# Kernel tuning notes

Hardware: AMD Instinct MI355X
Metric: run time of the kernel (lower is better)

Reference implementation:

```python
import jax, jax.numpy as jnp
import numpy as np

N_NODES = 50000
N_EDGES = 300000
HID = 256


def setup_inputs() -> dict:
    key = jax.random.key(0)
    ks = jax.random.split(key, 8)
    s = lambda fan_in: 1.0 / np.sqrt(fan_in)
    return {
        "node_embeddings": jax.random.normal(ks[0], (N_NODES, HID), dtype=jnp.float32),
        "edge_index": jax.random.randint(ks[1], (2, N_EDGES), 0, N_NODES, dtype=jnp.int64),
        "edge_attr": jax.random.normal(ks[2], (N_EDGES, 3), dtype=jnp.float32),
        "W1": jax.random.normal(ks[3], (2 * HID + 3, HID), dtype=jnp.float32) * s(2 * HID + 3),
        "b1": jnp.zeros((HID,), dtype=jnp.float32),
        "W2": jax.random.normal(ks[4], (HID, HID // 2), dtype=jnp.float32) * s(HID),
        "b2": jnp.zeros((HID // 2,), dtype=jnp.float32),
        "W3": jax.random.normal(ks[5], (HID // 2, HID // 4), dtype=jnp.float32) * s(HID // 2),
        "b3": jnp.zeros((HID // 4,), dtype=jnp.float32),
        "W4": jax.random.normal(ks[6], (HID // 4, 3), dtype=jnp.float32) * s(HID // 4),
        "b4": jnp.zeros((3,), dtype=jnp.float32),
    }


def reference(node_embeddings, edge_index, edge_attr, W1, b1, W2, b2, W3, b3, W4, b4):
    # Gather source/target node embeddings: [E, H] each
    src = node_embeddings[edge_index[0]]
    dst = node_embeddings[edge_index[1]]
    feats = jnp.concatenate([src, dst, edge_attr], axis=-1)  # [E, 2H+3]
    # edge_encoder: Linear -> ReLU -> (Dropout=identity in eval) -> Linear
    h = jax.nn.relu(feats @ W1 + b1)
    h = h @ W2 + b2  # [E, H//2]
    # classifier: Linear -> ReLU -> Linear
    h = jax.nn.relu(h @ W3 + b3)
    logits = h @ W4 + b4  # [E, 3]
    return logits
```

## Files before the change

kernel.cpp:

```cpp
#include <hip/hip_runtime.h>
#include <hip/hip_bf16.h>
#include <stdint.h>
#include <stddef.h>


#define NN 50000
#define NE 300000
#define KG(kq,g2) ((kq)*2+(g2))
#define NBG1 391

using bf16x8 = __attribute__((ext_vector_type(8))) short;
using f32x16 = __attribute__((ext_vector_type(16))) float;
using f32x4  = __attribute__((ext_vector_type(4))) float;
using f32x2  = __attribute__((ext_vector_type(2))) float;
using u32x4  = __attribute__((ext_vector_type(4))) unsigned int;
using u32x2  = __attribute__((ext_vector_type(2))) unsigned int;

#define OFF_PQ   0ULL
#define SZ_PQ    (50000ULL*512ULL*2ULL)
#define OFF_W1   (OFF_PQ + SZ_PQ)
#define SZ_W1    (512ULL*256ULL*2ULL)
#define OFF_W1C  (OFF_W1 + SZ_W1)
#define SZ_W1C   (3ULL*256ULL*4ULL)
#define OFF_W2   (OFF_W1C + SZ_W1C)
#define SZ_W2    (128ULL*256ULL*2ULL)
#define OFF_W3   (OFF_W2 + SZ_W2)
#define SZ_W3    (64ULL*128ULL*2ULL)
#define OFF_W4   (OFF_W3 + SZ_W3)
#define SZ_W4    (16ULL*64ULL*2ULL)
#define OFF_FLAG (OFF_W4 + SZ_W4)
#define WS_NEED  (OFF_FLAG + 16ULL)

__device__ __forceinline__ unsigned short f2bf(float x){
  unsigned u = __float_as_uint(x);
  unsigned r = 0x7FFFu + ((u >> 16) & 1u);
  return (unsigned short)((u + r) >> 16);
}
__device__ __forceinline__ unsigned cvtpk(float lo, float hi){
  unsigned r;
  asm("v_cvt_pk_bf16_f32 %0, %1, %2" : "=v"(r) : "v"(lo), "v"(hi));
  return r;
}
__device__ __forceinline__ f32x2 unpk(unsigned w){
  f32x2 r;
  r[0] = __uint_as_float(w << 16);
  r[1] = __uint_as_float(w & 0xFFFF0000u);
  return r;
}
__device__ __forceinline__ f32x16 mfma32(bf16x8 a, bf16x8 b, f32x16 c){
  return __builtin_amdgcn_mfma_f32_32x32x16_bf16(a, b, c, 0, 0, 0);
}
__device__ __forceinline__ f32x4 mfma16(bf16x8 a, bf16x8 b, f32x4 c){
  return __builtin_amdgcn_mfma_f32_16x16x32_bf16(a, b, c, 0, 0, 0);
}
__device__ __forceinline__ f32x16 zero16(){
  f32x16 v;
#pragma unroll
  for (int i = 0; i < 16; ++i) v[i] = 0.f;
  return v;
}

__global__ void prep_pack(const float* __restrict__ W1,
                          const int* __restrict__ ei32, char* __restrict__ ws)
{
  int i = blockIdx.x * 256 + threadIdx.x;
  unsigned short* w1i = (unsigned short*)(ws + OFF_W1);
  if (i < 131072){
    int out = i & 511;
    int kgj = i >> 9;
    int kg = kgj >> 3, j = kgj & 7;
    int k = (kg >> 1)*16 + (kg & 1)*8 + j;
    float v = (out < 256) ? W1[(size_t)k*256 + out]
                          : W1[(size_t)(256 + k)*256 + (out - 256)];
    w1i[((size_t)kg*512 + out)*8 + j] = f2bf(v);
  }
  if (i == 0){
    int f = 1;
    for (int t = 1; t < 64; t += 2) if (ei32[t] != 0) { f = 0; break; }
    *(int*)(ws + OFF_FLAG) = f;
  }
}

__global__ __launch_bounds__(512, 2) void gemm1(const float* __restrict__ emb,
                                                const float* __restrict__ b1,
                                                const float* __restrict__ W1,
                                                const float* __restrict__ W2,
                                                const float* __restrict__ W3,
                                                const float* __restrict__ W4,
                                                char* __restrict__ ws)
{
  __shared__ __align__(16) unsigned short U[16896];

  const int tid = threadIdx.x;
  const int bid = blockIdx.x;

  if (bid >= NBG1){
    int p = (bid - NBG1)*512 + tid;
    unsigned short* w2i = (unsigned short*)(ws + OFF_W2);
    unsigned short* w3i = (unsigned short*)(ws + OFF_W3);
    unsigned short* w4i = (unsigned short*)(ws + OFF_W4);
    float* w1c = (float*)(ws + OFF_W1C);
    if (p < 32768){
      int j = p & 7, out = (p >> 3) & 127, sg = p >> 10;
      int k = (sg >> 2)*32 + (sg & 3)*8 + j;
      w2i[p] = f2bf(W2[(size_t)k*128 + out]);
    } else if (p < 40960){
      int i3 = p - 32768;
      int j = i3 & 7, out = (i3 >> 3) & 63, sg = i3 >> 9;
      int k = (sg >> 2)*32 + (sg & 3)*8 + j;
      w3i[i3] = f2bf(W3[(size_t)k*64 + out]);
    } else if (p < 41984){
      int i4 = p - 40960;
      int j = i4 & 7, out = (i4 >> 3) & 15, sg = i4 >> 7;
      int k = (sg >> 2)*32 + (sg & 3)*8 + j;
      w4i[i4] = (out < 3) ? f2bf(W4[(size_t)k*3 + out]) : (unsigned short)0;
    } else if (p < 42752){
      int i5 = p - 41984;
      w1c[i5] = W1[(size_t)(512 + i5/256)*256 + (i5 & 255)];
    }
    return;
  }

  const int wv = tid >> 6, l = tid & 63, ln = l & 31, g2 = l >> 5;
  const int ob = wv * 64;
  const unsigned short* w1L = (const unsigned short*)(ws + OFF_W1);
  unsigned short* PQ = (unsigned short*)(ws + OFF_PQ);

  bf16x8 aw[2][16];
#pragma unroll
  for (int kq = 0; kq < 16; ++kq){
#pragma unroll
    for (int t2 = 0; t2 < 2; ++t2)
      aw[t2][kq] = *(const bf16x8*)(w1L + ((size_t)KG(kq,g2)*512 + ob + t2*32 + ln)*8);
  }

#pragma unroll 1
  for (int rep = 0; rep < 2; ++rep){
    const int nb = (bid*2 + rep) * 64;
    __syncthreads();

#pragma unroll
    for (int it = 0; it < 8; ++it){
      int u = it*512 + tid;
      int kg = u >> 7, node = (u >> 1) & 63, half = u & 1;
      int n = nb + node; if (n >= NN) n = NN - 1;
      int k = (kg >> 1)*16 + (kg & 1)*8 + half*4;
      f32x4 e = *(const f32x4*)(emb + (size_t)n*256 + k);
      u32x2 w; w[0] = cvtpk(e[0], e[1]); w[1] = cvtpk(e[2], e[3]);
      *(u32x2*)(U + (size_t)kg*512 + node*8 + half*4) = w;
    }
    __syncthreads();

    f32x16 acc[2][2];
    acc[0][0] = zero16(); acc[0][1] = zero16();
    acc[1][0] = zero16(); acc[1][1] = zero16();
#pragma unroll
    for (int kq = 0; kq < 16; ++kq){
      bf16x8 b0  = *(const bf16x8*)(U + ((size_t)KG(kq,g2)*64 +      ln)*8);
      bf16x8 b1v = *(const bf16x8*)(U + ((size_t)KG(kq,g2)*64 + 32 + ln)*8);
      acc[0][0] = mfma32(aw[0][kq], b0,  acc[0][0]);
      acc[1][0] = mfma32(aw[1][kq], b0,  acc[1][0]);
      acc[0][1] = mfma32(aw[0][kq], b1v, acc[0][1]);
      acc[1][1] = mfma32(aw[1][kq], b1v, acc[1][1]);
    }
    __syncthreads();

    const int r_ = tid >> 4;
    const int j_ = tid & 15;
#define G1PASS(BG)                                                             \
    {                                                                          \
      _Pragma("unroll")                                                        \
      for (int t2 = 0; t2 < 2; ++t2){                                          \
        _Pragma("unroll")                                                      \
        for (int rr = 0; rr < 4; ++rr){                                        \
          int o = ob + t2*32 + rr*8 + g2*4;                                    \
          f32x4 bv = {0.f,0.f,0.f,0.f};                                        \
          if (ob + t2*32 < 256) bv = *(const f32x4*)(b1 + o);                  \
          unsigned d0 = cvtpk(acc[t2][BG][rr*4+0]+bv[0], acc[t2][BG][rr*4+1]+bv[1]); \
          unsigned d1 = cvtpk(acc[t2][BG][rr*4+2]+bv[2], acc[t2][BG][rr*4+3]+bv[3]); \
          u32x2 st = {d0, d1};                                                 \
          *(u32x2*)(U + (size_t)ln*516 + o) = st;                              \
        }                                                                      \
      }                                                                        \
      __syncthreads();                                                         \
      {                                                                        \
        int n = nb + (BG)*32 + r_;                                             \
        if (n < NN){                                                           \
          _Pragma("unroll")                                                    \
          for (int ii = 0; ii < 4; ++ii){                                      \
            uint4 v = *(const uint4*)(U + (size_t)r_*516 + ii*128 + j_*8);     \
            *(uint4*)(PQ + (size_t)n*512 + ii*128 + j_*8) = v;                 \
          }                                                                    \
        }                                                                      \
      }                                                                        \
    }
    G1PASS(0);
    __syncthreads();
    G1PASS(1);
#undef G1PASS
  }
}


#define PAIRX(LO, HI, D) ((D)==0 ? (f32x2){(LO)[0],(LO)[1]} : \
                          (D)==1 ? (f32x2){(LO)[2],(LO)[3]} : \
                          (D)==2 ? (f32x2){(HI)[0],(HI)[1]} : \
                                   (f32x2){(HI)[2],(HI)[3]})

#define H1BUILD(PC, QC, A0, A1, A2, BOUT)                                      \
  {                                                                            \
    u32x4 pu = __builtin_bit_cast(u32x4, PC);                                  \
    u32x4 qu = __builtin_bit_cast(u32x4, QC);                                  \
    f32x2 z2 = {0.f, 0.f};                                                     \
    unsigned bu0, bu1, bu2, bu3;                                               \
    _Pragma("unroll")                                                          \
    for (int d = 0; d < 4; ++d){                                               \
      f32x2 h = unpk(pu[d]) + unpk(qu[d]);                                     \
      h += PAIRX(w0lo, w0hi, d) * (A0);                                        \
      h += PAIRX(w1lo, w1hi, d) * (A1);                                        \
      h += PAIRX(w2lo, w2hi, d) * (A2);                                        \
      h = __builtin_elementwise_max(h, z2);                                    \
      unsigned c = cvtpk(h[0], h[1]);                                          \
      if (d==0) bu0 = c; else if (d==1) bu1 = c; else if (d==2) bu2 = c;       \
      else bu3 = c;                                                            \
    }                                                                          \
    u32x4 buv = {bu0, bu1, bu2, bu3};                                          \
    BOUT = __builtin_bit_cast(bf16x8, buv);                                    \
  }

#define L2S(S, P0, Q0, P1, Q1)                                                 \
  {                                                                            \
    const int kb = (S)*32 + g4*8;                                              \
    f32x4 w0lo = *(const f32x4*)(w1c_lds +   0 + kb);                          \
    f32x4 w0hi = *(const f32x4*)(w1c_lds +   4 + kb);                          \
    f32x4 w1lo = *(const f32x4*)(w1c_lds + 256 + kb);                          \
    f32x4 w1hi = *(const f32x4*)(w1c_lds + 260 + kb);                          \
    f32x4 w2lo = *(const f32x4*)(w1c_lds + 512 + kb);                          \
    f32x4 w2hi = *(const f32x4*)(w1c_lds + 516 + kb);                          \
    bf16x8 b0, b1;                                                             \
    H1BUILD(P0, Q0, at0e0, at1e0, at2e0, b0);                                  \
    H1BUILD(P1, Q1, at0e1, at1e1, at2e1, b1);                                  \
    if ((S) + 2 <= 7){                                                         \
      P0 = *(const bf16x8*)(Prow0 + ((S)+2)*32);                               \
      Q0 = *(const bf16x8*)(Qrow0 + ((S)+2)*32);                               \
      P1 = *(const bf16x8*)(Prow1 + ((S)+2)*32);                               \
      Q1 = *(const bf16x8*)(Qrow1 + ((S)+2)*32);                               \
    }                                                                          \
    const char* abase = smem + (size_t)((S)*4 + g4)*2048 + c16*16;             \
    _Pragma("unroll")                                                          \
    for (int t = 0; t < 8; ++t){                                               \
      bf16x8 af = *(const bf16x8*)(abase + t*256);                             \
      acc2[t][0] = mfma16(af, b0, acc2[t][0]);                                 \
      acc2[t][1] = mfma16(af, b1, acc2[t][1]);                                 \
    }                                                                          \
  }

__global__ __launch_bounds__(512, 4) void fused(const int* __restrict__ eidx,
                                                const float* __restrict__ attr,
                                                const float* __restrict__ b2,
                                                const float* __restrict__ b3,
                                                const float* __restrict__ b4,
                                                const char* __restrict__ ws,
                                                float* __restrict__ out)
{
  __shared__ __align__(16) char smem[65536 + 3072];
  const int tid = threadIdx.x;
  const int wv = tid >> 6, l = tid & 63, c16 = l & 15, g4 = l >> 4;

  const unsigned short* PQ  = (const unsigned short*)(ws + OFF_PQ);
  const unsigned short* w3g = (const unsigned short*)(ws + OFF_W3);
  const unsigned short* w4g = (const unsigned short*)(ws + OFF_W4);
  const float* W1c = (const float*)(ws + OFF_W1C);
  const int flag64 = *(const int*)(ws + OFF_FLAG);
  const float* w1c_lds = (const float*)(smem + 65536);

  const int ebase = blockIdx.x * 256 + wv * 32;
  const int e0 = ebase + c16,      e1 = ebase + 16 + c16;
  const bool ev0 = (e0 < NE),      ev1 = (e1 < NE);
  const int ec0 = ev0 ? e0 : 0,    ec1 = ev1 ? e1 : 0;
  const int si0 = flag64 ? eidx[2*(size_t)ec0]        : eidx[ec0];
  const int di0 = flag64 ? eidx[2*((size_t)NE + ec0)] : eidx[NE + ec0];
  const int si1 = flag64 ? eidx[2*(size_t)ec1]        : eidx[ec1];
  const int di1 = flag64 ? eidx[2*((size_t)NE + ec1)] : eidx[NE + ec1];

  const float at0e0 = ev0 ? attr[(size_t)ec0*3 + 0] : 0.f;
  const float at1e0 = ev0 ? attr[(size_t)ec0*3 + 1] : 0.f;
  const float at2e0 = ev0 ? attr[(size_t)ec0*3 + 2] : 0.f;
  const float at0e1 = ev1 ? attr[(size_t)ec1*3 + 0] : 0.f;
  const float at1e1 = ev1 ? attr[(size_t)ec1*3 + 1] : 0.f;
  const float at2e1 = ev1 ? attr[(size_t)ec1*3 + 2] : 0.f;

  const unsigned short* Prow0 = PQ + (size_t)si0*512 + g4*8;
  const unsigned short* Qrow0 = PQ + (size_t)di0*512 + 256 + g4*8;
  const unsigned short* Prow1 = PQ + (size_t)si1*512 + g4*8;
  const unsigned short* Qrow1 = PQ + (size_t)di1*512 + 256 + g4*8;

  bf16x8 pA0 = *(const bf16x8*)(Prow0 +  0), qA0 = *(const bf16x8*)(Qrow0 +  0);
  bf16x8 pA1 = *(const bf16x8*)(Prow1 +  0), qA1 = *(const bf16x8*)(Qrow1 +  0);
  bf16x8 pB0 = *(const bf16x8*)(Prow0 + 32), qB0 = *(const bf16x8*)(Qrow0 + 32);
  bf16x8 pB1 = *(const bf16x8*)(Prow1 + 32), qB1 = *(const bf16x8*)(Qrow1 + 32);

  {
    const uint4* src = (const uint4*)(ws + OFF_W2);
    uint4* dst = (uint4*)smem;
#pragma unroll
    for (int it = 0; it < 8; ++it) dst[it*512 + tid] = src[it*512 + tid];
    if (tid < 192) ((f32x4*)(smem + 65536))[tid] = ((const f32x4*)W1c)[tid];
  }
  __syncthreads();

  f32x4 acc2[8][2];
#pragma unroll
  for (int t = 0; t < 8; ++t){ acc2[t][0] = (f32x4){0,0,0,0}; acc2[t][1] = (f32x4){0,0,0,0}; }

  L2S(0, pA0, qA0, pA1, qA1);
  L2S(1, pB0, qB0, pB1, qB1);
  L2S(2, pA0, qA0, pA1, qA1);
  L2S(3, pB0, qB0, pB1, qB1);
  L2S(4, pA0, qA0, pA1, qA1);
  L2S(5, pB0, qB0, pB1, qB1);
  L2S(6, pA0, qA0, pA1, qA1);
  L2S(7, pB0, qB0, pB1, qB1);

  __syncthreads();

  unsigned short* hslot = (unsigned short*)(smem + wv*8192);
#pragma unroll
  for (int t = 0; t < 8; ++t){
    f32x4 bv = *(const f32x4*)(b2 + t*16 + g4*4);
    const int sg_o = t*2 + (g4 >> 1);
    const int j0 = (g4 & 1)*4;
#pragma unroll
    for (int g = 0; g < 2; ++g){
      unsigned d0 = cvtpk(acc2[t][g][0]+bv[0], acc2[t][g][1]+bv[1]);
      unsigned d1 = cvtpk(acc2[t][g][2]+bv[2], acc2[t][g][3]+bv[3]);
      u32x2 st = {d0, d1};
      *(u32x2*)(hslot + ((sg_o*32 + g*16 + c16)*8 + j0)) = st;
    }
  }

  f32x4 acc3[4][2];
#pragma unroll
  for (int t = 0; t < 4; ++t){ acc3[t][0] = (f32x4){0,0,0,0}; acc3[t][1] = (f32x4){0,0,0,0}; }
#pragma unroll
  for (int ks = 0; ks < 4; ++ks){
    const int sg = ks*4 + g4;
    bf16x8 bb0 = *(const bf16x8*)(hslot + (sg*32 +      c16)*8);
    bf16x8 bb1 = *(const bf16x8*)(hslot + (sg*32 + 16 + c16)*8);
#pragma unroll
    for (int t = 0; t < 4; ++t){
      bf16x8 af = *(const bf16x8*)(w3g + ((size_t)sg*64 + t*16 + c16)*8);
      acc3[t][0] = mfma16(af, bb0, acc3[t][0]);
      acc3[t][1] = mfma16(af, bb1, acc3[t][1]);
    }
  }

#pragma unroll
  for (int t = 0; t < 4; ++t){
    f32x4 bv = *(const f32x4*)(b3 + t*16 + g4*4);
    const int sg_o = t*2 + (g4 >> 1);
    const int j0 = (g4 & 1)*4;
#pragma unroll
    for (int g = 0; g < 2; ++g){
      unsigned d0 = cvtpk(fmaxf(acc3[t][g][0]+bv[0],0.f), fmaxf(acc3[t][g][1]+bv[1],0.f));
      unsigned d1 = cvtpk(fmaxf(acc3[t][g][2]+bv[2],0.f), fmaxf(acc3[t][g][3]+bv[3],0.f));
      u32x2 st = {d0, d1};
      *(u32x2*)(hslot + ((sg_o*32 + g*16 + c16)*8 + j0)) = st;
    }
  }

  f32x4 acc40 = {0,0,0,0}, acc41 = {0,0,0,0};
#pragma unroll
  for (int ks = 0; ks < 2; ++ks){
    const int sg = ks*4 + g4;
    bf16x8 af = *(const bf16x8*)(w4g + ((size_t)sg*16 + c16)*8);
    bf16x8 bb0 = *(const bf16x8*)(hslot + (sg*32 +      c16)*8);
    bf16x8 bb1 = *(const bf16x8*)(hslot + (sg*32 + 16 + c16)*8);
    acc40 = mfma16(af, bb0, acc40);
    acc41 = mfma16(af, bb1, acc41);
  }
  if (g4 == 0){
    float c0 = b4[0], c1 = b4[1], c2 = b4[2];
    if (ev0){
      out[(size_t)e0*3 + 0] = acc40[0] + c0;
      out[(size_t)e0*3 + 1] = acc40[1] + c1;
      out[(size_t)e0*3 + 2] = acc40[2] + c2;
    }
    if (ev1){
      out[(size_t)e1*3 + 0] = acc41[0] + c0;
      out[(size_t)e1*3 + 1] = acc41[1] + c1;
      out[(size_t)e1*3 + 2] = acc41[2] + c2;
    }
  }
}

extern "C" void kernel_launch(void* const* d_in, const int* in_sizes, int n_in,
                              void* d_out, int out_size, void* d_ws, size_t ws_size,
                              hipStream_t stream)
{
  const float* emb  = (const float*)d_in[0];
  const int*   eidx = (const int*)  d_in[1];
  const float* attr = (const float*)d_in[2];
  const float* W1   = (const float*)d_in[3];
  const float* b1   = (const float*)d_in[4];
  const float* W2   = (const float*)d_in[5];
  const float* b2   = (const float*)d_in[6];
  const float* W3   = (const float*)d_in[7];
  const float* b3   = (const float*)d_in[8];
  const float* W4   = (const float*)d_in[9];
  const float* b4   = (const float*)d_in[10];
  char* ws = (char*)d_ws;
  float* out = (float*)d_out;

  if (ws_size < WS_NEED) return;

  prep_pack<<<512, 256, 0, stream>>>(W1, eidx, ws);
  gemm1<<<NBG1 + 84, 512, 0, stream>>>(emb, b1, W1, W2, W3, W4, ws);
  fused<<<(NE + 255)/256, 512, 0, stream>>>(eidx, attr, b2, b3, b4, ws, out);
}
```

Measured before the change: 113.2 us.

## Process one node tile per block and stream W1 fragments to raise occupancy

The gemm1 kernel no longer preloads all 32 W1 fragments into registers and loops over two node tiles. Each block now handles a single 64-node tile, so there are twice as many blocks, and W1 fragments are double-buffered from global memory inside the unrolled MFMA loop. Launch bounds are raised to allow 4 blocks per CU. The goal is lower register pressure, higher occupancy and better latency hiding, at the cost of re-reading W1 from L2 for every block and losing reuse of the weights across tiles.

```diff
diff --git a/kernel.cpp b/kernel.cpp
--- a/kernel.cpp
+++ b/kernel.cpp
@@ -7,7 +7,7 @@
 #define NN 50000
 #define NE 300000
 #define KG(kq,g2) ((kq)*2+(g2))
-#define NBG1 391
+#define NBG1 782
 
 using bf16x8 = __attribute__((ext_vector_type(8))) short;
 using f32x16 = __attribute__((ext_vector_type(16))) float;
@@ -81,7 +81,7 @@
   }
 }
 
-__global__ __launch_bounds__(512, 2) void gemm1(const float* __restrict__ emb,
+__global__ __launch_bounds__(512, 4) void gemm1(const float* __restrict__ emb,
                                                 const float* __restrict__ b1,
                                                 const float* __restrict__ W1,
                                                 const float* __restrict__ W2,
@@ -123,82 +123,99 @@
 
   const int wv = tid >> 6, l = tid & 63, ln = l & 31, g2 = l >> 5;
   const int ob = wv * 64;
+  const int nb = bid * 64;
   const unsigned short* w1L = (const unsigned short*)(ws + OFF_W1);
   unsigned short* PQ = (unsigned short*)(ws + OFF_PQ);
 
-  bf16x8 aw[2][16];
-#pragma unroll
-  for (int kq = 0; kq < 16; ++kq){
-#pragma unroll
-    for (int t2 = 0; t2 < 2; ++t2)
-      aw[t2][kq] = *(const bf16x8*)(w1L + ((size_t)KG(kq,g2)*512 + ob + t2*32 + ln)*8);
-  }
-
-#pragma unroll 1
-  for (int rep = 0; rep < 2; ++rep){
-    const int nb = (bid*2 + rep) * 64;
-    __syncthreads();
-
-#pragma unroll
-    for (int it = 0; it < 8; ++it){
-      int u = it*512 + tid;
-      int kg = u >> 7, node = (u >> 1) & 63, half = u & 1;
-      int n = nb + node; if (n >= NN) n = NN - 1;
-      int k = (kg >> 1)*16 + (kg & 1)*8 + half*4;
-      f32x4 e = *(const f32x4*)(emb + (size_t)n*256 + k);
-      u32x2 w; w[0] = cvtpk(e[0], e[1]); w[1] = cvtpk(e[2], e[3]);
-      *(u32x2*)(U + (size_t)kg*512 + node*8 + half*4) = w;
-    }
-    __syncthreads();
-
-    f32x16 acc[2][2];
-    acc[0][0] = zero16(); acc[0][1] = zero16();
-    acc[1][0] = zero16(); acc[1][1] = zero16();
-#pragma unroll
-    for (int kq = 0; kq < 16; ++kq){
-      bf16x8 b0  = *(const bf16x8*)(U + ((size_t)KG(kq,g2)*64 +      ln)*8);
-      bf16x8 b1v = *(const bf16x8*)(U + ((size_t)KG(kq,g2)*64 + 32 + ln)*8);
-      acc[0][0] = mfma32(aw[0][kq], b0,  acc[0][0]);
-      acc[1][0] = mfma32(aw[1][kq], b0,  acc[1][0]);
-      acc[0][1] = mfma32(aw[0][kq], b1v, acc[0][1]);
-      acc[1][1] = mfma32(aw[1][kq], b1v, acc[1][1]);
-    }
-    __syncthreads();
-
-    const int r_ = tid >> 4;
-    const int j_ = tid & 15;
+#pragma unroll
+  for (int it = 0; it < 8; ++it){
+    int u = it*512 + tid;
+    int kg = u >> 7, node = (u >> 1) & 63, half = u & 1;
+    int n = nb + node; if (n >= NN) n = NN - 1;
+    int k = (kg >> 1)*16 + (kg & 1)*8 + half*4;
+    f32x4 e = *(const f32x4*)(emb + (size_t)n*256 + k);
+    u32x2 w; w[0] = cvtpk(e[0], e[1]); w[1] = cvtpk(e[2], e[3]);
+    *(u32x2*)(U + (size_t)kg*512 + node*8 + half*4) = w;
+  }
+
+  bf16x8 awA0 = *(const bf16x8*)(w1L + ((size_t)KG(0,g2)*512 + ob +      ln)*8);
+  bf16x8 awA1 = *(const bf16x8*)(w1L + ((size_t)KG(0,g2)*512 + ob + 32 + ln)*8);
+  bf16x8 awB0 = *(const bf16x8*)(w1L + ((size_t)KG(1,g2)*512 + ob +      ln)*8);
+  bf16x8 awB1 = *(const bf16x8*)(w1L + ((size_t)KG(1,g2)*512 + ob + 32 + ln)*8);
+
+  __syncthreads();
+
+  f32x16 acc[2][2];
+  acc[0][0] = zero16(); acc[0][1] = zero16();
+  acc[1][0] = zero16(); acc[1][1] = zero16();
+
+#define G1STEP(KQ, W0, W1F)                                                    \
+  {                                                                            \
+    bf16x8 b0  = *(const bf16x8*)(U + ((size_t)KG(KQ,g2)*64 +      ln)*8);     \
+    bf16x8 b1v = *(const bf16x8*)(U + ((size_t)KG(KQ,g2)*64 + 32 + ln)*8);     \
+    bf16x8 a0 = W0, a1 = W1F;                                                  \
+    if ((KQ) + 2 <= 15){                                                       \
+      W0  = *(const bf16x8*)(w1L + ((size_t)KG((KQ)+2,g2)*512 + ob +      ln)*8); \
+      W1F = *(const bf16x8*)(w1L + ((size_t)KG((KQ)+2,g2)*512 + ob + 32 + ln)*8); \
+    }                                                                          \
+    acc[0][0] = mfma32(a0, b0,  acc[0][0]);                                    \
+    acc[1][0] = mfma32(a1, b0,  acc[1][0]);                                    \
+    acc[0][1] = mfma32(a0, b1v, acc[0][1]);                                    \
+    acc[1][1] = mfma32(a1, b1v, acc[1][1]);                                    \
+  }
+  G1STEP(0,  awA0, awA1);
+  G1STEP(1,  awB0, awB1);
+  G1STEP(2,  awA0, awA1);
+  G1STEP(3,  awB0, awB1);
+  G1STEP(4,  awA0, awA1);
+  G1STEP(5,  awB0, awB1);
+  G1STEP(6,  awA0, awA1);
+  G1STEP(7,  awB0, awB1);
+  G1STEP(8,  awA0, awA1);
+  G1STEP(9,  awB0, awB1);
+  G1STEP(10, awA0, awA1);
+  G1STEP(11, awB0, awB1);
+  G1STEP(12, awA0, awA1);
+  G1STEP(13, awB0, awB1);
+  G1STEP(14, awA0, awA1);
+  G1STEP(15, awB0, awB1);
+#undef G1STEP
+
+  __syncthreads();
+
+  const int r_ = tid >> 4;
+  const int j_ = tid & 15;
 #define G1PASS(BG)                                                             \
+  {                                                                            \
+    _Pragma("unroll")                                                          \
+    for (int t2 = 0; t2 < 2; ++t2){                                            \
+      _Pragma("unroll")                                                        \
+      for (int rr = 0; rr < 4; ++rr){                                          \
+        int o = ob + t2*32 + rr*8 + g2*4;                                      \
+        f32x4 bv = {0.f,0.f,0.f,0.f};                                          \
+        if (ob + t2*32 < 256) bv = *(const f32x4*)(b1 + o);                    \
+        unsigned d0 = cvtpk(acc[t2][BG][rr*4+0]+bv[0], acc[t2][BG][rr*4+1]+bv[1]); \
+        unsigned d1 = cvtpk(acc[t2][BG][rr*4+2]+bv[2], acc[t2][BG][rr*4+3]+bv[3]); \
+        u32x2 st = {d0, d1};                                                   \
+        *(u32x2*)(U + (size_t)ln*516 + o) = st;                                \
+      }                                                                        \
+    }                                                                          \
+    __syncthreads();                                                           \
     {                                                                          \
-      _Pragma("unroll")                                                        \
-      for (int t2 = 0; t2 < 2; ++t2){                                          \
+      int n = nb + (BG)*32 + r_;                                               \
+      if (n < NN){                                                             \
         _Pragma("unroll")                                                      \
-        for (int rr = 0; rr < 4; ++rr){                                        \
-          int o = ob + t2*32 + rr*8 + g2*4;                                    \
-          f32x4 bv = {0.f,0.f,0.f,0.f};                                        \
-          if (ob + t2*32 < 256) bv = *(const f32x4*)(b1 + o);                  \
-          unsigned d0 = cvtpk(acc[t2][BG][rr*4+0]+bv[0], acc[t2][BG][rr*4+1]+bv[1]); \
-          unsigned d1 = cvtpk(acc[t2][BG][rr*4+2]+bv[2], acc[t2][BG][rr*4+3]+bv[3]); \
-          u32x2 st = {d0, d1};                                                 \
-          *(u32x2*)(U + (size_t)ln*516 + o) = st;                              \
+        for (int ii = 0; ii < 4; ++ii){                                        \
+          uint4 v = *(const uint4*)(U + (size_t)r_*516 + ii*128 + j_*8);       \
+          *(uint4*)(PQ + (size_t)n*512 + ii*128 + j_*8) = v;                   \
         }                                                                      \
       }                                                                        \
-      __syncthreads();                                                         \
-      {                                                                        \
-        int n = nb + (BG)*32 + r_;                                             \
-        if (n < NN){                                                           \
-          _Pragma("unroll")                                                    \
-          for (int ii = 0; ii < 4; ++ii){                                      \
-            uint4 v = *(const uint4*)(U + (size_t)r_*516 + ii*128 + j_*8);     \
-            *(uint4*)(PQ + (size_t)n*512 + ii*128 + j_*8) = v;                 \
-          }                                                                    \
-        }                                                                      \
-      }                                                                        \
-    }
-    G1PASS(0);
-    __syncthreads();
-    G1PASS(1);
+    }                                                                          \
+  }
+  G1PASS(0);
+  __syncthreads();
+  G1PASS(1);
 #undef G1PASS
-  }
 }
 
 
```

Measured after the change: 107.1 us (median of 2 runs). 5.3% less time.
